# Optimization experiments

Measured on AMD Instinct MI355X. Metric: run time of the kernel, lower is better.

Reference implementation:

```python
import jax, jax.numpy as jnp
import numpy as np

DECAY = 0.8
EPS = 1e-05


def setup_inputs() -> dict:
    key = jax.random.key(0)
    k_x, k_e = jax.random.split(key)
    x = jax.random.normal(k_x, (8, 4096, 256), dtype=jnp.float32)
    embed = jax.random.normal(k_e, (8192, 256), dtype=jnp.float32)
    cluster_size = jnp.zeros((8192,), dtype=jnp.float32)
    embed_avg = embed  # buffer initialized as embed.clone()
    return {"x": x, "embed": embed, "cluster_size": cluster_size, "embed_avg": embed_avg}


def reference(x, embed, cluster_size, embed_avg):
    shape = x.shape
    K, d = embed.shape
    flatten = x.reshape(-1, d)  # [N, d]

    dist = -(jnp.sum(flatten * flatten, axis=1, keepdims=True)
             - 2.0 * (flatten @ embed.T)
             + jnp.sum(embed * embed, axis=1)[None, :])  # [N, K]
    embed_ind = jnp.argmax(dist, axis=-1)  # [N]

    quantize = jnp.take(embed, embed_ind, axis=0).reshape(shape)
    embed_ind_out = embed_ind.reshape(shape[:-1])

    # Training-mode EMA update (one_hot sum / one_hot matmul expressed as scatter-adds)
    counts = jnp.zeros((K,), dtype=x.dtype).at[embed_ind].add(1.0)  # embed_onehot.sum(0)
    embed_sum = jnp.zeros((K, d), dtype=x.dtype).at[embed_ind].add(flatten)  # (flatten^T @ onehot)^T

    new_cluster_size = cluster_size * DECAY + counts * (1.0 - DECAY)
    new_embed_avg = embed_avg * DECAY + embed_sum * (1.0 - DECAY)

    smoothed = (new_cluster_size + EPS) / (new_cluster_size.sum() + K * EPS) * new_cluster_size.sum()
    new_embed = new_embed_avg / smoothed[:, None]

    return quantize, embed_ind_out, new_cluster_size, new_embed_avg, new_embed
```

## Files before the change

kernel.cpp:

```cpp
#include <hip/hip_runtime.h>

#define N_ROWS 32768
#define DIM    256
#define KCODES 8192
#define DECAYF 0.8f
#define OMDF   0.2f
#define EPSF   1e-5f

#define Q_OFF    0
#define IND_OFF  8388608
#define CS_OFF   8421376
#define EA_OFF   8429568
#define NE_OFF   10526720


#define WS_E2   0
#define WS_SUM  40960

typedef _Float16 half8 __attribute__((ext_vector_type(8)));
typedef float floatx16 __attribute__((ext_vector_type(16)));

#define GLOAD16(g, l) __builtin_amdgcn_global_load_lds( \
    (const __attribute__((address_space(1))) void*)(g), \
    (__attribute__((address_space(3))) void*)(l), 16, 0, 0)

__global__ void zero1_kernel(const float* __restrict__ cs,
                             float* __restrict__ out, float* __restrict__ ws) {
  __shared__ float red[4];
  const int t = threadIdx.x;
  int g = blockIdx.x * blockDim.x + t;
  unsigned long long* gbest = (unsigned long long*)(out + EA_OFF);
  gbest[g] = 0ULL;
  if (g < KCODES) out[CS_OFF + g] = 0.0f;
  const int nq = (KCODES * DIM) / 4;
  float4* ne4 = (float4*)(out + NE_OFF);
  for (int i = g; i < nq; i += gridDim.x * blockDim.x)
    ne4[i] = make_float4(0.f, 0.f, 0.f, 0.f);
  if (blockIdx.x == 0) {
    float s = 0.0f;
    for (int j = t; j < KCODES; j += 256) s += cs[j];
    #pragma unroll
    for (int o = 32; o; o >>= 1) s += __shfl_xor(s, o);
    if ((t & 63) == 0) red[t >> 6] = s;
    __syncthreads();
    if (t == 0) ws[WS_SUM] = red[0] + red[1] + red[2] + red[3];
  }
}

#define PREP_ROWS 32
__global__ void prep_x_kernel(const float* __restrict__ x,
                              _Float16* __restrict__ Xp) {
  __shared__ __align__(16) _Float16 L[PREP_ROWS][264];
  const int t = threadIdx.x;
  const int row0 = blockIdx.x * PREP_ROWS;
  #pragma unroll
  for (int it = 0; it < 8; ++it) {
    int idx = it * 256 + t;
    int r = idx >> 6, q = idx & 63;
    float4 v = *(const float4*)&x[(size_t)(row0 + r) * DIM + q * 4];
    L[r][q * 4 + 0] = (_Float16)v.x;
    L[r][q * 4 + 1] = (_Float16)v.y;
    L[r][q * 4 + 2] = (_Float16)v.z;
    L[r][q * 4 + 3] = (_Float16)v.w;
  }
  __syncthreads();
  #pragma unroll
  for (int it = 0; it < 4; ++it) {
    int idx = it * 256 + t;
    int slot = idx >> 5, r = idx & 31;
    *(float4*)&Xp[((size_t)slot * N_ROWS + row0 + r) * 8] =
        *(const float4*)&L[r][slot * 8];
  }
}

__global__ void prep_e_kernel(const float* __restrict__ embed,
                              _Float16* __restrict__ Ep,
                              float* __restrict__ e2) {
  __shared__ __align__(16) _Float16 L[PREP_ROWS][264];
  const int t = threadIdx.x;
  const int row0 = blockIdx.x * PREP_ROWS;
  #pragma unroll
  for (int it = 0; it < 8; ++it) {
    int idx = it * 256 + t;
    int r = idx >> 6, q = idx & 63;
    float4 v = *(const float4*)&embed[(size_t)(row0 + r) * DIM + q * 4];
    L[r][q * 4 + 0] = (_Float16)v.x;
    L[r][q * 4 + 1] = (_Float16)v.y;
    L[r][q * 4 + 2] = (_Float16)v.z;
    L[r][q * 4 + 3] = (_Float16)v.w;
    float ssq = v.x * v.x + v.y * v.y + v.z * v.z + v.w * v.w;
    #pragma unroll
    for (int o = 32; o; o >>= 1) ssq += __shfl_xor(ssq, o);
    if ((t & 63) == 0) e2[row0 + r] = ssq;
  }
  __syncthreads();
  #pragma unroll
  for (int it = 0; it < 4; ++it) {
    int idx = it * 256 + t;
    int slot = idx >> 5, r = idx & 31;
    *(float4*)&Ep[((size_t)slot * KCODES + row0 + r) * 8] =
        *(const float4*)&L[r][slot * 8];
  }
}

__global__ __launch_bounds__(512, 2) void main_kernel(
    const _Float16* __restrict__ Xp, const _Float16* __restrict__ Ep,
    const float* __restrict__ e2, unsigned long long* __restrict__ gbest) {
  __shared__ __align__(16) _Float16 As[4 * 4 * 256 * 8];
  __shared__ __align__(16) _Float16 Bs[4 * 4 * 256 * 8];
  __shared__ __align__(16) float e2s[256];

  const int t = threadIdx.x;
  const int w = t >> 6;
  const int lane = t & 63;
  const int l31 = lane & 31;
  const int h = lane >> 5;
  const int wm = w >> 2;
  const int wn = w & 3;

  const int bid = blockIdx.x;
  const int bi = bid >> 3;
  const int cb = (bid & 7) * 4 + (bi >> 5);
  const int rbg = bi & 31;
  const int codes0 = cb * 256;
  const int rowbase = rbg * 1024;

  const bool isA = (w < 4);
  const int slot = isA ? w : (w - 4);

  auto stage = [&](int s) {
    const int buf = s & 3;
    const int se = (s & 7) * 4 + slot;
    if (isA) {
      const _Float16* src = Ep + ((size_t)se * KCODES + codes0 + lane) * 8;
      _Float16* dst = &As[buf * 8192 + slot * 2048];
      #pragma unroll
      for (int q = 0; q < 4; ++q)
        GLOAD16(src + q * 512, dst + q * 512);
    } else {
      const int row0 = rowbase + (s >> 3) * 256;
      const _Float16* src = Xp + ((size_t)se * N_ROWS + row0 + lane) * 8;
      _Float16* dst = &Bs[buf * 8192 + slot * 2048];
      #pragma unroll
      for (int q = 0; q < 4; ++q)
        GLOAD16(src + q * 512, dst + q * 512);
    }
  };

  if (t < 64) {
    float4 v = *(const float4*)&e2[codes0 + t * 4];
    *(float4*)&e2s[t * 4] = v;
  }
  __builtin_amdgcn_sched_barrier(0);
  stage(0);
  stage(1);
  asm volatile("s_waitcnt vmcnt(4)" ::: "memory");
  asm volatile("s_waitcnt lgkmcnt(0)" ::: "memory");
  __builtin_amdgcn_s_barrier();
  __builtin_amdgcn_sched_barrier(0);

  floatx16 acc[4][2];
  unsigned long long pbest[4][2];

  #pragma unroll
  for (int tile = 0; tile < 4; ++tile) {
    #pragma unroll
    for (int ct = 0; ct < 4; ++ct) {
      const int cl = wm * 128 + ct * 32 + 4 * h;
      #pragma unroll
      for (int rq = 0; rq < 4; ++rq) {
        float4 v = *(const float4*)&e2s[cl + rq * 8];
        acc[ct][0][rq * 4 + 0] = -0.5f * v.x;
        acc[ct][0][rq * 4 + 1] = -0.5f * v.y;
        acc[ct][0][rq * 4 + 2] = -0.5f * v.z;
        acc[ct][0][rq * 4 + 3] = -0.5f * v.w;
      }
      acc[ct][1] = acc[ct][0];
    }

    #pragma unroll 1
    for (int i = 0; i < 8; ++i) {
      const int s = tile * 8 + i;
      if (s + 2 < 32) stage(s + 2);
      __builtin_amdgcn_sched_barrier(0);

      const int cur = (i & 3) * 8192;
      #pragma unroll
      for (int ks = 0; ks < 2; ++ks) {
        const int sbase = cur + (2 * ks + h) * 2048;
        half8 a0 = *(const half8*)&As[sbase + (wm * 128 + l31) * 8];
        half8 a1 = *(const half8*)&As[sbase + (wm * 128 + 32 + l31) * 8];
        half8 a2 = *(const half8*)&As[sbase + (wm * 128 + 64 + l31) * 8];
        half8 a3 = *(const half8*)&As[sbase + (wm * 128 + 96 + l31) * 8];
        half8 b0 = *(const half8*)&Bs[sbase + (wn * 64 + l31) * 8];
        half8 b1 = *(const half8*)&Bs[sbase + (wn * 64 + 32 + l31) * 8];
        __builtin_amdgcn_s_setprio(1);
        acc[0][0] = __builtin_amdgcn_mfma_f32_32x32x16_f16(a0, b0, acc[0][0], 0, 0, 0);
        acc[0][1] = __builtin_amdgcn_mfma_f32_32x32x16_f16(a0, b1, acc[0][1], 0, 0, 0);
        acc[1][0] = __builtin_amdgcn_mfma_f32_32x32x16_f16(a1, b0, acc[1][0], 0, 0, 0);
        acc[1][1] = __builtin_amdgcn_mfma_f32_32x32x16_f16(a1, b1, acc[1][1], 0, 0, 0);
        acc[2][0] = __builtin_amdgcn_mfma_f32_32x32x16_f16(a2, b0, acc[2][0], 0, 0, 0);
        acc[2][1] = __builtin_amdgcn_mfma_f32_32x32x16_f16(a2, b1, acc[2][1], 0, 0, 0);
        acc[3][0] = __builtin_amdgcn_mfma_f32_32x32x16_f16(a3, b0, acc[3][0], 0, 0, 0);
        acc[3][1] = __builtin_amdgcn_mfma_f32_32x32x16_f16(a3, b1, acc[3][1], 0, 0, 0);
        __builtin_amdgcn_s_setprio(0);
      }
      __builtin_amdgcn_sched_barrier(0);

      if (s < 31) {
        if (s < 30) {
          asm volatile("s_waitcnt vmcnt(4)" ::: "memory");
        } else {
          asm volatile("s_waitcnt vmcnt(0)" ::: "memory");
        }
        __builtin_amdgcn_s_barrier();
        __builtin_amdgcn_sched_barrier(0);
      }
    }

    #pragma unroll
    for (int rt = 0; rt < 2; ++rt) {
      float best = -3.0e38f;
      int bidx = 0;
      #pragma unroll
      for (int ct = 0; ct < 4; ++ct) {
        const int cbase = codes0 + wm * 128 + ct * 32 + 4 * h;
        #pragma unroll
        for (int r = 0; r < 16; ++r) {
          const int code = cbase + (r & 3) + 8 * (r >> 2);
          float v = acc[ct][rt][r];
          if (v > best || (v == best && code < bidx)) { best = v; bidx = code; }
        }
      }
      unsigned u = __float_as_uint(best);
      u = (u & 0x80000000u) ? ~u : (u | 0x80000000u);
      unsigned long long p =
          ((unsigned long long)u << 32) | (unsigned)(8191 - bidx);
      unsigned long long op = (unsigned long long)__shfl_xor((long long)p, 32);
      if (op > p) p = op;
      pbest[tile][rt] = p;
    }
  }

  #pragma unroll
  for (int tile = 0; tile < 4; ++tile)
    #pragma unroll
    for (int rt = 0; rt < 2; ++rt)
      if (h == 0)
        atomicMax(&gbest[rowbase + tile * 256 + wn * 64 + rt * 32 + l31],
                  pbest[tile][rt]);
}

__global__ void finish_rows_kernel(const float* __restrict__ x,
                                   const float* __restrict__ embed,
                                   const unsigned long long* __restrict__ gbest,
                                   float* __restrict__ out) {
  const int total = N_ROWS * (DIM / 4);
  for (int it = blockIdx.x * blockDim.x + threadIdx.x; it < total;
       it += gridDim.x * blockDim.x) {
    int row = it >> 6;
    int q = it & 63;
    unsigned long long p = gbest[row];
    int k = 8191 - (int)(unsigned)(p & 0xFFFFFFFFull);
    float4 ev = *(const float4*)&embed[(size_t)k * DIM + q * 4];
    *(float4*)&out[Q_OFF + (size_t)row * DIM + q * 4] = ev;
    float4 xv = *(const float4*)&x[(size_t)row * DIM + q * 4];
    float* es = out + NE_OFF + (size_t)k * DIM + q * 4;
    atomicAdd(es + 0, xv.x);
    atomicAdd(es + 1, xv.y);
    atomicAdd(es + 2, xv.z);
    atomicAdd(es + 3, xv.w);
    if (q == 0) {
      out[IND_OFF + row] = (float)k;
      atomicAdd(&out[CS_OFF + k], 1.0f);
    }
  }
}

__global__ void final_kernel(const float* __restrict__ cs,
                             const float* __restrict__ embed_avg,
                             float* __restrict__ out,
                             const float* __restrict__ ws_sum) {
  const float S = DECAYF * (*ws_sum) + OMDF * (float)N_ROWS;
  const float scale = S / (S + (float)KCODES * EPSF);
  const int total = (KCODES * DIM) / 4;
  for (int it = blockIdx.x * blockDim.x + threadIdx.x; it < total;
       it += gridDim.x * blockDim.x) {
    int k = it >> 6;
    int q = it & 63;
    float cnt = out[CS_OFF + k];
    float ncs = cs[k] * DECAYF + cnt * OMDF;
    if (q == 0) out[CS_OFF + k] = ncs;
    float4 ea = *(const float4*)&embed_avg[(size_t)it * 4];
    float4 es = *(const float4*)&out[NE_OFF + (size_t)it * 4];
    float4 nea;
    nea.x = ea.x * DECAYF + es.x * OMDF;
    nea.y = ea.y * DECAYF + es.y * OMDF;
    nea.z = ea.z * DECAYF + es.z * OMDF;
    nea.w = ea.w * DECAYF + es.w * OMDF;
    *(float4*)&out[EA_OFF + (size_t)it * 4] = nea;
    float inv_sm = 1.0f / ((ncs + EPSF) * scale);
    float4 ne;
    ne.x = nea.x * inv_sm;
    ne.y = nea.y * inv_sm;
    ne.z = nea.z * inv_sm;
    ne.w = nea.w * inv_sm;
    *(float4*)&out[NE_OFF + (size_t)it * 4] = ne;
  }
}

extern "C" void kernel_launch(void* const* d_in, const int* in_sizes, int n_in,
                              void* d_out, int out_size, void* d_ws, size_t ws_size,
                              hipStream_t stream) {
  const float* x = (const float*)d_in[0];
  const float* embed = (const float*)d_in[1];
  const float* cs = (const float*)d_in[2];
  const float* ea = (const float*)d_in[3];
  float* out = (float*)d_out;
  float* ws = (float*)d_ws;

  float* e2 = ws + WS_E2;
  float* ws_sum = ws + WS_SUM;

  _Float16* Xp = (_Float16*)(out + Q_OFF);
  unsigned long long* gbest = (unsigned long long*)(out + EA_OFF);
  _Float16* Ep = (_Float16*)(out + EA_OFF + 65536);

  zero1_kernel<<<128, 256, 0, stream>>>(cs, out, ws);
  prep_x_kernel<<<N_ROWS / PREP_ROWS, 256, 0, stream>>>(x, Xp);
  prep_e_kernel<<<KCODES / PREP_ROWS, 256, 0, stream>>>(embed, Ep, e2);
  main_kernel<<<1024, 512, 0, stream>>>(Xp, Ep, e2, gbest);
  finish_rows_kernel<<<2048, 256, 0, stream>>>(x, embed, gbest, out);
  final_kernel<<<2048, 256, 0, stream>>>(cs, ea, out, ws_sum);
}
```

Measured before the change: 439.7 us.

## Replace float atomic scatter-add with counting-sort bucketed per-code summation

Replaces per-element float atomicAdd scatter of x rows into embed_sum with a counting sort: count rows per code, prefix-scan offsets, scatter row indices into buckets, then one wave per code sums its rows and writes directly. This removes the zeroing of the 8 MB embed_sum buffer and the heavy float atomic contention. It adds three small kernels, including a single-block prefix scan, and makes work imbalanced when codes have very uneven row counts. Summation becomes deterministic apart from the order in which rows land in each bucket.

```diff
diff --git a/kernel.cpp b/kernel.cpp
--- a/kernel.cpp
+++ b/kernel.cpp
@@ -14,8 +14,11 @@
 #define NE_OFF   10526720
 
 
-#define WS_E2   0
-#define WS_SUM  40960
+#define WS_E2    0
+#define WS_CNT   8192
+#define WS_START 16384
+#define WS_CUR   24576
+#define WS_SUM   40960
 
 typedef _Float16 half8 __attribute__((ext_vector_type(8)));
 typedef float floatx16 __attribute__((ext_vector_type(16)));
@@ -31,11 +34,7 @@
   int g = blockIdx.x * blockDim.x + t;
   unsigned long long* gbest = (unsigned long long*)(out + EA_OFF);
   gbest[g] = 0ULL;
-  if (g < KCODES) out[CS_OFF + g] = 0.0f;
-  const int nq = (KCODES * DIM) / 4;
-  float4* ne4 = (float4*)(out + NE_OFF);
-  for (int i = g; i < nq; i += gridDim.x * blockDim.x)
-    ne4[i] = make_float4(0.f, 0.f, 0.f, 0.f);
+  if (g < KCODES) ((int*)(ws + WS_CNT))[g] = 0;
   if (blockIdx.x == 0) {
     float s = 0.0f;
     for (int j = t; j < KCODES; j += 256) s += cs[j];
@@ -251,62 +250,110 @@
                   pbest[tile][rt]);
 }
 
-__global__ void finish_rows_kernel(const float* __restrict__ x,
-                                   const float* __restrict__ embed,
-                                   const unsigned long long* __restrict__ gbest,
-                                   float* __restrict__ out) {
-  const int total = N_ROWS * (DIM / 4);
-  for (int it = blockIdx.x * blockDim.x + threadIdx.x; it < total;
-       it += gridDim.x * blockDim.x) {
-    int row = it >> 6;
-    int q = it & 63;
+__global__ void finish_q_kernel(const float* __restrict__ embed,
+                                const unsigned long long* __restrict__ gbest,
+                                float* __restrict__ out, int* __restrict__ cnt) {
+  const int lane = threadIdx.x & 63;
+  const int wave = (blockIdx.x * blockDim.x + threadIdx.x) >> 6;
+  for (int row = wave; row < N_ROWS; row += 2048) {
     unsigned long long p = gbest[row];
     int k = 8191 - (int)(unsigned)(p & 0xFFFFFFFFull);
-    float4 ev = *(const float4*)&embed[(size_t)k * DIM + q * 4];
-    *(float4*)&out[Q_OFF + (size_t)row * DIM + q * 4] = ev;
-    float4 xv = *(const float4*)&x[(size_t)row * DIM + q * 4];
-    float* es = out + NE_OFF + (size_t)k * DIM + q * 4;
-    atomicAdd(es + 0, xv.x);
-    atomicAdd(es + 1, xv.y);
-    atomicAdd(es + 2, xv.z);
-    atomicAdd(es + 3, xv.w);
-    if (q == 0) {
+    float4 ev = *(const float4*)&embed[(size_t)k * DIM + lane * 4];
+    *(float4*)&out[Q_OFF + (size_t)row * DIM + lane * 4] = ev;
+    if (lane == 0) {
       out[IND_OFF + row] = (float)k;
-      atomicAdd(&out[CS_OFF + k], 1.0f);
-    }
-  }
-}
-
-__global__ void final_kernel(const float* __restrict__ cs,
-                             const float* __restrict__ embed_avg,
-                             float* __restrict__ out,
-                             const float* __restrict__ ws_sum) {
+      atomicAdd(&cnt[k], 1);
+    }
+  }
+}
+
+__global__ void prefix_kernel(const int* __restrict__ cnt,
+                              int* __restrict__ start,
+                              int* __restrict__ cursor) {
+  __shared__ int part[1024];
+  const int t = threadIdx.x;
+  int loc[8];
+  int s = 0;
+  #pragma unroll
+  for (int j = 0; j < 8; ++j) { loc[j] = cnt[t * 8 + j]; s += loc[j]; }
+  part[t] = s;
+  __syncthreads();
+  for (int off = 1; off < 1024; off <<= 1) {
+    int v = (t >= off) ? part[t - off] : 0;
+    __syncthreads();
+    part[t] += v;
+    __syncthreads();
+  }
+  int base = part[t] - s;
+  #pragma unroll
+  for (int j = 0; j < 8; ++j) {
+    start[t * 8 + j] = base;
+    cursor[t * 8 + j] = base;
+    base += loc[j];
+  }
+}
+
+__global__ void scatter_rows_kernel(const float* __restrict__ out,
+                                    int* __restrict__ cursor,
+                                    int* __restrict__ rowlist) {
+  int r = blockIdx.x * blockDim.x + threadIdx.x;
+  int k = (int)out[IND_OFF + r];
+  int pos = atomicAdd(&cursor[k], 1);
+  rowlist[pos] = r;
+}
+
+__global__ void bucket_sum_kernel(const float* __restrict__ x,
+                                  const float* __restrict__ cs,
+                                  const int* __restrict__ start,
+                                  const int* __restrict__ cnt,
+                                  const int* __restrict__ rowlist,
+                                  float* __restrict__ out) {
+  const int lane = threadIdx.x & 63;
+  const int k = blockIdx.x * 4 + (threadIdx.x >> 6);
+  const int s = start[k];
+  const int n = cnt[k];
+  float4 acc = make_float4(0.f, 0.f, 0.f, 0.f);
+  int i = 0;
+  for (; i + 2 <= n; i += 2) {
+    int r0 = rowlist[s + i];
+    int r1 = rowlist[s + i + 1];
+    float4 v0 = *(const float4*)&x[(size_t)r0 * DIM + lane * 4];
+    float4 v1 = *(const float4*)&x[(size_t)r1 * DIM + lane * 4];
+    acc.x += v0.x + v1.x; acc.y += v0.y + v1.y;
+    acc.z += v0.z + v1.z; acc.w += v0.w + v1.w;
+  }
+  if (i < n) {
+    int r0 = rowlist[s + i];
+    float4 v0 = *(const float4*)&x[(size_t)r0 * DIM + lane * 4];
+    acc.x += v0.x; acc.y += v0.y; acc.z += v0.z; acc.w += v0.w;
+  }
+  *(float4*)&out[NE_OFF + (size_t)k * DIM + lane * 4] = acc;
+  if (lane == 0) out[CS_OFF + k] = cs[k] * DECAYF + (float)n * OMDF;
+}
+
+__global__ void final2_kernel(const float* __restrict__ embed_avg,
+                              float* __restrict__ out,
+                              const float* __restrict__ ws_sum) {
   const float S = DECAYF * (*ws_sum) + OMDF * (float)N_ROWS;
   const float scale = S / (S + (float)KCODES * EPSF);
-  const int total = (KCODES * DIM) / 4;
-  for (int it = blockIdx.x * blockDim.x + threadIdx.x; it < total;
-       it += gridDim.x * blockDim.x) {
-    int k = it >> 6;
-    int q = it & 63;
-    float cnt = out[CS_OFF + k];
-    float ncs = cs[k] * DECAYF + cnt * OMDF;
-    if (q == 0) out[CS_OFF + k] = ncs;
-    float4 ea = *(const float4*)&embed_avg[(size_t)it * 4];
-    float4 es = *(const float4*)&out[NE_OFF + (size_t)it * 4];
-    float4 nea;
-    nea.x = ea.x * DECAYF + es.x * OMDF;
-    nea.y = ea.y * DECAYF + es.y * OMDF;
-    nea.z = ea.z * DECAYF + es.z * OMDF;
-    nea.w = ea.w * DECAYF + es.w * OMDF;
-    *(float4*)&out[EA_OFF + (size_t)it * 4] = nea;
-    float inv_sm = 1.0f / ((ncs + EPSF) * scale);
-    float4 ne;
-    ne.x = nea.x * inv_sm;
-    ne.y = nea.y * inv_sm;
-    ne.z = nea.z * inv_sm;
-    ne.w = nea.w * inv_sm;
-    *(float4*)&out[NE_OFF + (size_t)it * 4] = ne;
-  }
+  int it = blockIdx.x * blockDim.x + threadIdx.x;
+  int k = it >> 6;
+  float ncs = out[CS_OFF + k];
+  float4 ea = *(const float4*)&embed_avg[(size_t)it * 4];
+  float4 es = *(const float4*)&out[NE_OFF + (size_t)it * 4];
+  float4 nea;
+  nea.x = ea.x * DECAYF + es.x * OMDF;
+  nea.y = ea.y * DECAYF + es.y * OMDF;
+  nea.z = ea.z * DECAYF + es.z * OMDF;
+  nea.w = ea.w * DECAYF + es.w * OMDF;
+  *(float4*)&out[EA_OFF + (size_t)it * 4] = nea;
+  float inv_sm = 1.0f / ((ncs + EPSF) * scale);
+  float4 ne;
+  ne.x = nea.x * inv_sm;
+  ne.y = nea.y * inv_sm;
+  ne.z = nea.z * inv_sm;
+  ne.w = nea.w * inv_sm;
+  *(float4*)&out[NE_OFF + (size_t)it * 4] = ne;
 }
 
 extern "C" void kernel_launch(void* const* d_in, const int* in_sizes, int n_in,
@@ -320,16 +367,23 @@
   float* ws = (float*)d_ws;
 
   float* e2 = ws + WS_E2;
+  int* cnt = (int*)(ws + WS_CNT);
+  int* start = (int*)(ws + WS_START);
+  int* cursor = (int*)(ws + WS_CUR);
   float* ws_sum = ws + WS_SUM;
 
   _Float16* Xp = (_Float16*)(out + Q_OFF);
   unsigned long long* gbest = (unsigned long long*)(out + EA_OFF);
+  int* rowlist = (int*)(out + EA_OFF);
   _Float16* Ep = (_Float16*)(out + EA_OFF + 65536);
 
   zero1_kernel<<<128, 256, 0, stream>>>(cs, out, ws);
   prep_x_kernel<<<N_ROWS / PREP_ROWS, 256, 0, stream>>>(x, Xp);
   prep_e_kernel<<<KCODES / PREP_ROWS, 256, 0, stream>>>(embed, Ep, e2);
   main_kernel<<<1024, 512, 0, stream>>>(Xp, Ep, e2, gbest);
-  finish_rows_kernel<<<2048, 256, 0, stream>>>(x, embed, gbest, out);
-  final_kernel<<<2048, 256, 0, stream>>>(cs, ea, out, ws_sum);
-}
+  finish_q_kernel<<<512, 256, 0, stream>>>(embed, gbest, out, cnt);
+  prefix_kernel<<<1, 1024, 0, stream>>>(cnt, start, cursor);
+  scatter_rows_kernel<<<128, 256, 0, stream>>>(out, cursor, rowlist);
+  bucket_sum_kernel<<<2048, 256, 0, stream>>>(x, cs, start, cnt, rowlist, out);
+  final2_kernel<<<2048, 256, 0, stream>>>(ea, out, ws_sum);
+}
```

Result: faster. 389.2 us (-11.5%).
